# Optimization experiments

Measured on AMD Instinct MI355X. Metric: run time of the kernel, lower is better.

The kernel has to match this reference:

```python
import jax, jax.numpy as jnp
import numpy as np

DIM = 1024
NUM_HEADS = 16
HEAD_DIM = DIM // NUM_HEADS
ROPE_BASE = 10000.0


def apply_rope(x, pos):
    """x: [B, H, N, D] float32, pos: [B, N] int -> rotated x (rotate-half convention)."""
    d = x.shape[-1]
    # inv_freq: [D/2]
    inv_freq = 1.0 / (ROPE_BASE ** (jnp.arange(0, d, 2, dtype=jnp.float32) / d))
    # angles: [B, 1, N, D/2]
    ang = pos.astype(jnp.float32)[:, None, :, None] * inv_freq
    cos = jnp.concatenate([jnp.cos(ang), jnp.cos(ang)], axis=-1)
    sin = jnp.concatenate([jnp.sin(ang), jnp.sin(ang)], axis=-1)
    x1, x2 = x[..., : d // 2], x[..., d // 2 :]
    rotated = jnp.concatenate([-x2, x1], axis=-1)
    return x * cos + rotated * sin


def setup_inputs() -> dict:
    key = jax.random.key(0)
    ks = jax.random.split(key, 10)
    B, Nq, Nk, C = 4, 512, 2048, DIM
    scale = 0.02
    inp = {
        "query": jax.random.normal(ks[0], (B, Nq, C), dtype=jnp.float32),
        "key": jax.random.normal(ks[1], (B, Nk, C), dtype=jnp.float32),
        "value": jax.random.normal(ks[2], (B, Nk, C), dtype=jnp.float32),
        "qpos": jnp.sort(jax.random.randint(ks[3], (B, Nq), 0, Nk, dtype=jnp.int32), axis=-1),
        "kpos": jnp.sort(jax.random.randint(ks[4], (B, Nk), 0, Nk, dtype=jnp.int32), axis=-1),
        # learned params (qkv_bias=False; output proj has bias, per nn.Linear default)
        "Wq": jax.random.normal(ks[5], (C, C), dtype=jnp.float32) * scale,
        "Wk": jax.random.normal(ks[6], (C, C), dtype=jnp.float32) * scale,
        "Wv": jax.random.normal(ks[7], (C, C), dtype=jnp.float32) * scale,
        "Wp": jax.random.normal(ks[8], (C, C), dtype=jnp.float32) * scale,
        "bp": jax.random.normal(ks[9], (C,), dtype=jnp.float32) * scale,
    }
    return inp


def reference(query, key, value, qpos, kpos, Wq, Wk, Wv, Wp, bp):
    B, Nq, C = query.shape
    Nk = key.shape[1]
    H, D = NUM_HEADS, C // NUM_HEADS
    scale = D ** (-0.5)

    # separate Q/K/V linear projections (bias=False), split heads -> [B, H, N, D]
    q = (query @ Wq.T).reshape(B, Nq, H, D).transpose(0, 2, 1, 3)
    k = (key @ Wk.T).reshape(B, Nk, H, D).transpose(0, 2, 1, 3)
    v = (value @ Wv.T).reshape(B, Nk, H, D).transpose(0, 2, 1, 3)

    # RoPE applied in fp32 (matches the cast-to-float/rotate/cast-back sequence)
    q = apply_rope(q.astype(jnp.float32), qpos).astype(query.dtype)
    k = apply_rope(k.astype(jnp.float32), kpos).astype(key.dtype)

    # scaled dot-product attention (dropout_p = 0.0, non-causal)
    scores = jnp.einsum("bhqd,bhkd->bhqk", q, k) * scale
    attn = jax.nn.softmax(scores, axis=-1)
    x = jnp.einsum("bhqk,bhkd->bhqd", attn, v)

    # merge heads and output projection (with bias)
    x = x.transpose(0, 2, 1, 3).reshape(B, Nq, C)
    x = x @ Wp.T + bp
    return x
```

## Files before the change

### kernel.cpp

```cpp
#include <hip/hip_runtime.h>
#include <math.h>

#define B_ 4
#define NQ 512
#define NK 2048
#define C_ 1024
#define H_ 16
#define D_ 64
#define KK 1024

typedef __attribute__((ext_vector_type(8))) _Float16 half8;
typedef __attribute__((ext_vector_type(4))) _Float16 half4;
typedef __attribute__((ext_vector_type(4))) float float4v;

__device__ __forceinline__ void g2l16(const _Float16* g, _Float16* l)
{
    __builtin_amdgcn_global_load_lds(
        (const __attribute__((address_space(1))) unsigned int*)g,
        (__attribute__((address_space(3))) unsigned int*)l, 16, 0, 0);
}

__global__ __launch_bounds__(256) void cvt_w4(const float* __restrict__ W0,
                                              const float* __restrict__ W1,
                                              const float* __restrict__ W2,
                                              const float* __restrict__ W3,
                                              _Float16* __restrict__ W16)
{
    const int w = blockIdx.x >> 10, row = blockIdx.x & 1023;
    const float* src = (w == 0) ? W0 : (w == 1) ? W1 : (w == 2) ? W2 : W3;
    const int col = threadIdx.x * 4;
    float4 f = *(const float4*)(src + (size_t)row * 1024 + col);
    half4 h;
    h[0] = (_Float16)f.x; h[1] = (_Float16)f.y;
    h[2] = (_Float16)f.z; h[3] = (_Float16)f.w;
    *(half4*)(W16 + ((size_t)w << 20) + (size_t)row * 1024 + col) = h;
}

__global__ __launch_bounds__(256) void cvt_qkv(const float* __restrict__ q,
                                               const float* __restrict__ k,
                                               const float* __restrict__ v,
                                               _Float16* __restrict__ xq,
                                               _Float16* __restrict__ xk,
                                               _Float16* __restrict__ xv)
{
    const int blk = blockIdx.x;
    const float* src; _Float16* dst; int row;
    if (blk < 2048)       { src = q; dst = xq; row = blk; }
    else if (blk < 10240) { src = k; dst = xk; row = blk - 2048; }
    else                  { src = v; dst = xv; row = blk - 10240; }
    const int col = threadIdx.x * 4;
    float4 f = *(const float4*)(src + (size_t)row * 1024 + col);
    half4 h;
    h[0] = (_Float16)f.x; h[1] = (_Float16)f.y;
    h[2] = (_Float16)f.z; h[3] = (_Float16)f.w;
    *(half4*)(dst + (size_t)row * 1024 + col) = h;
}

__device__ __forceinline__ void gemm_body(const _Float16* __restrict__ A,
                                          const _Float16* __restrict__ Bw,
                                          _Float16* __restrict__ Yh,
                                          float* __restrict__ Yf,
                                          int mode, int nsh,
                                          const float* __restrict__ bias,
                                          _Float16* sA, _Float16* sB)
{
    const int tid = threadIdx.x;
    const int lane = tid & 63, wave = tid >> 6;
    const int n0 = blockIdx.x * 128, m0 = blockIdx.y * 128;
    const int wm = (wave >> 1) * 64, wn = (wave & 1) * 64;
    const int fm = lane & 15, quad = lane >> 4;

    const int srow = wave * 32 + (lane >> 3);
    const int soct = (lane & 7) ^ (srow & 7);
    const _Float16* gA = A  + (size_t)(m0 + srow) * KK + soct * 8;
    const _Float16* gB = Bw + (size_t)(n0 + srow) * KK + soct * 8;

    float4v acc[4][4];
    #pragma unroll
    for (int i = 0; i < 4; ++i)
        #pragma unroll
        for (int j = 0; j < 4; ++j)
            #pragma unroll
            for (int e = 0; e < 4; ++e) acc[i][j][e] = 0.0f;

    for (int k0 = 0; k0 < KK; k0 += 64) {
        __syncthreads();
        #pragma unroll
        for (int u = 0; u < 4; ++u) {
            g2l16(gA + (size_t)u * 8 * KK + k0, &sA[(wave * 32 + u * 8) * 64]);
            g2l16(gB + (size_t)u * 8 * KK + k0, &sB[(wave * 32 + u * 8) * 64]);
        }
        __syncthreads();

        #pragma unroll
        for (int ks = 0; ks < 2; ++ks) {
            const int po = ((ks * 4 + quad) ^ (fm & 7)) * 8;
            half8 a[4], b[4];
            #pragma unroll
            for (int i = 0; i < 4; ++i) {
                a[i] = *(const half8*)&sA[(wm + i * 16 + fm) * 64 + po];
                b[i] = *(const half8*)&sB[(wn + i * 16 + fm) * 64 + po];
            }
            #pragma unroll
            for (int i = 0; i < 4; ++i)
                #pragma unroll
                for (int j = 0; j < 4; ++j)
                    acc[i][j] = __builtin_amdgcn_mfma_f32_16x16x32_f16(a[i], b[j], acc[i][j], 0, 0, 0);
        }
    }

    const int rr = quad * 4;
    if (mode == 0) {
        const int nmask = (1 << nsh) - 1;
        #pragma unroll
        for (int i = 0; i < 4; ++i)
            #pragma unroll
            for (int r = 0; r < 4; ++r) {
                const int m = m0 + wm + i * 16 + rr + r;
                const int b = m >> nsh, n = m & nmask;
                #pragma unroll
                for (int j = 0; j < 4; ++j) {
                    const int c = n0 + wn + j * 16 + fm;
                    Yh[((((size_t)b * H_ + (c >> 6)) << nsh) + n) * 64 + (c & 63)] = (_Float16)acc[i][j][r];
                }
            }
    } else if (mode == 2) {
        const int nmask = (1 << nsh) - 1;
        #pragma unroll
        for (int i = 0; i < 4; ++i)
            #pragma unroll
            for (int r = 0; r < 4; ++r) {
                const int m = m0 + wm + i * 16 + rr + r;
                const int b = m >> nsh, n = m & nmask;
                #pragma unroll
                for (int j = 0; j < 4; ++j) {
                    const int c = n0 + wn + j * 16 + fm;
                    Yh[(((size_t)(b * H_ + (c >> 6)) * 64) + (c & 63)) * NK + n] = (_Float16)acc[i][j][r];
                }
            }
    } else {
        #pragma unroll
        for (int i = 0; i < 4; ++i)
            #pragma unroll
            for (int r = 0; r < 4; ++r) {
                const int m = m0 + wm + i * 16 + rr + r;
                #pragma unroll
                for (int j = 0; j < 4; ++j) {
                    const int c = n0 + wn + j * 16 + fm;
                    Yf[(size_t)m * 1024 + c] = acc[i][j][r] + bias[c];
                }
            }
    }
}

__global__ __launch_bounds__(256) void gemm_qkv(const _Float16* __restrict__ xq,
                                                const _Float16* __restrict__ xk,
                                                const _Float16* __restrict__ xv,
                                                const _Float16* __restrict__ W16,
                                                _Float16* __restrict__ qhp,
                                                _Float16* __restrict__ khp,
                                                _Float16* __restrict__ vtp)
{
    __shared__ _Float16 sA[128 * 64];
    __shared__ _Float16 sB[128 * 64];
    const int z = blockIdx.z;
    if (z == 0)
        gemm_body(xk, W16 + (1u << 20), khp, nullptr, 0, 11, nullptr, sA, sB);
    else if (z == 1)
        gemm_body(xv, W16 + (2u << 20), vtp, nullptr, 2, 11, nullptr, sA, sB);
    else {
        if (blockIdx.y >= 16) return;
        gemm_body(xq, W16, qhp, nullptr, 0, 9, nullptr, sA, sB);
    }
}

__global__ __launch_bounds__(256) void gemm_out(const _Float16* __restrict__ A,
                                                const _Float16* __restrict__ Bw,
                                                float* __restrict__ Yf,
                                                const float* __restrict__ bias)
{
    __shared__ _Float16 sA[128 * 64];
    __shared__ _Float16 sB[128 * 64];
    gemm_body(A, Bw, nullptr, Yf, 1, 0, bias, sA, sB);
}

__global__ __launch_bounds__(256) void rope_qk(_Float16* __restrict__ qh,
                                               _Float16* __restrict__ kh,
                                               const int* __restrict__ qpos,
                                               const int* __restrict__ kpos)
{
    int idx = blockIdx.x * 256 + threadIdx.x;
    const int QTOT = B_ * H_ * NQ * 32;
    _Float16* t; const int* pos; int Nseq; float scale;
    if (idx < QTOT) { t = qh; pos = qpos; Nseq = NQ; scale = 0.125f; }
    else { idx -= QTOT; t = kh; pos = kpos; Nseq = NK; scale = 1.0f; }

    const int i = idx & 31;
    const int n = (idx >> 5) % Nseq;
    const int b = (idx / (32 * Nseq)) >> 4;

    const double r = 0.74989420933245582;
    double f = 1.0;
    for (int u = 0; u < i; ++u) f *= r;

    const double ang = (double)pos[b * Nseq + n] * f;
    const double TWO_PI = 6.2831853071795864769;
    const float red = (float)(ang - TWO_PI * floor(ang / TWO_PI));
    float s, c;
    sincosf(red, &s, &c);

    const size_t base = ((size_t)(idx >> 5)) * 64 + i;
    const float x1 = (float)t[base];
    const float x2 = (float)t[base + 32];
    t[base]      = (_Float16)((x1 * c - x2 * s) * scale);
    t[base + 32] = (_Float16)((x2 * c + x1 * s) * scale);
}

__global__ __launch_bounds__(512) void attn_fused(const _Float16* __restrict__ qh,
                                                  const _Float16* __restrict__ kh,
                                                  const _Float16* __restrict__ vt,
                                                  _Float16* __restrict__ xw16)
{
    __shared__ _Float16 sK[2][64 * 64];
    __shared__ _Float16 sV[2][64 * 64];
    __shared__ _Float16 ps[8][16][66];

    const int tid = threadIdx.x;
    const int lane = tid & 63, wv = tid >> 6;
    const int bhi = blockIdx.x & 63;
    const int qquad = blockIdx.x >> 6;
    const size_t bh = (size_t)bhi;
    const int qt = qquad * 8 + wv;

    const int fm = lane & 15;
    const int quad = lane >> 4;
    const int fq = quad * 8;

    const _Float16* kb = kh + bh * NK * 64;
    const _Float16* vb = vt + bh * (size_t)64 * NK;

    const int r0 = lane >> 3;
    const int c4 = lane & 7;
    const int sch = c4 ^ r0;
    const _Float16* gK = kb + (size_t)(wv * 8 + r0) * 64 + sch * 8;
    const _Float16* gV = vb + (size_t)(wv * 8 + r0) * NK + sch * 8;

    const _Float16* qb = qh + (bh * NQ + (size_t)qt * 16) * 64;
    half8 aq[2];
    aq[0] = *(const half8*)(qb + (size_t)fm * 64 + fq);
    aq[1] = *(const half8*)(qb + (size_t)fm * 64 + 32 + fq);

    float l_acc[4] = {};
    float4v O[4];
    #pragma unroll
    for (int j = 0; j < 4; ++j)
        #pragma unroll
        for (int e = 0; e < 4; ++e) O[j][e] = 0.0f;

    const float4v z4 = {0.0f, 0.0f, 0.0f, 0.0f};

    g2l16(gK, &sK[0][wv * 512]);
    g2l16(gV, &sV[0][wv * 512]);
    __syncthreads();

    for (int it = 0; it < 32; ++it) {
        const int cur = it & 1;
        if (it < 31) {
            g2l16(gK + (size_t)(it + 1) * 64 * 64, &sK[cur ^ 1][wv * 512]);
            g2l16(gV + (it + 1) * 64,              &sV[cur ^ 1][wv * 512]);
        }
        const _Float16* Kc = sK[cur];
        const _Float16* Vc = sV[cur];

        half8 bk[4][2];
        #pragma unroll
        for (int j = 0; j < 4; ++j)
            #pragma unroll
            for (int ks = 0; ks < 2; ++ks)
                bk[j][ks] = *(const half8*)&Kc[(j * 16 + fm) * 64 + (((ks * 4 + quad) ^ (fm & 7)) * 8)];

        float4v s[4];
        __builtin_amdgcn_s_setprio(1);
        #pragma unroll
        for (int j = 0; j < 4; ++j) {
            s[j] = __builtin_amdgcn_mfma_f32_16x16x32_f16(aq[0], bk[j][0], z4, 0, 0, 0);
            s[j] = __builtin_amdgcn_mfma_f32_16x16x32_f16(aq[1], bk[j][1], s[j], 0, 0, 0);
        }
        __builtin_amdgcn_s_setprio(0);

        half8 bv[4][2];
        #pragma unroll
        for (int j = 0; j < 4; ++j)
            #pragma unroll
            for (int ks = 0; ks < 2; ++ks)
                bv[j][ks] = *(const half8*)&Vc[(j * 16 + fm) * 64 + (((ks * 4 + quad) ^ (fm & 7)) * 8)];

        #pragma unroll
        for (int j = 0; j < 4; ++j)
            #pragma unroll
            for (int r = 0; r < 4; ++r) {
                const float p = __expf(s[j][r]);
                l_acc[r] += p;
                ps[wv][quad * 4 + r][16 * j + fm] = (_Float16)p;
            }

        __builtin_amdgcn_s_setprio(1);
        #pragma unroll
        for (int ks = 0; ks < 2; ++ks) {
            half8 pa = *(const half8*)&ps[wv][fm][ks * 32 + fq];
            #pragma unroll
            for (int j = 0; j < 4; ++j)
                O[j] = __builtin_amdgcn_mfma_f32_16x16x32_f16(pa, bv[j][ks], O[j], 0, 0, 0);
        }
        __builtin_amdgcn_s_setprio(0);

        __syncthreads();
    }

    #pragma unroll
    for (int r = 0; r < 4; ++r) {
        float l = l_acc[r];
        l += __shfl_xor(l, 1);
        l += __shfl_xor(l, 2);
        l += __shfl_xor(l, 4);
        l += __shfl_xor(l, 8);
        const float inv = 1.0f / l;
        const int qr = quad * 4 + r;
        const int row = (bhi >> 4) * 512 + qt * 16 + qr;
        #pragma unroll
        for (int j = 0; j < 4; ++j) {
            const int col = (bhi & 15) * 64 + j * 16 + fm;
            xw16[(size_t)row * 1024 + col] = (_Float16)(O[j][r] * inv);
        }
    }
}

extern "C" void kernel_launch(void* const* d_in, const int* in_sizes, int n_in,
                              void* d_out, int out_size, void* d_ws, size_t ws_size,
                              hipStream_t stream)
{
    const float* query = (const float*)d_in[0];
    const float* key   = (const float*)d_in[1];
    const float* value = (const float*)d_in[2];
    const int*   qpos  = (const int*)d_in[3];
    const int*   kpos  = (const int*)d_in[4];
    const float* Wq    = (const float*)d_in[5];
    const float* Wk    = (const float*)d_in[6];
    const float* Wv    = (const float*)d_in[7];
    const float* Wp    = (const float*)d_in[8];
    const float* bp    = (const float*)d_in[9];
    float* out = (float*)d_out;

    char* ws = (char*)d_ws;
    _Float16* xk16  = (_Float16*)(ws);
    _Float16* xv16  = (_Float16*)(ws + (16u << 20));
    _Float16* xq16  = (_Float16*)(ws + (32u << 20));
    _Float16* W16   = (_Float16*)(ws + (36u << 20));
    _Float16* qhp   = (_Float16*)(ws + (44u << 20));
    _Float16* khp   = (_Float16*)(ws + (48u << 20));
    _Float16* vtp   = (_Float16*)(ws + (64u << 20));

    cvt_w4 <<<4096, 256, 0, stream>>>(Wq, Wk, Wv, Wp, W16);
    cvt_qkv<<<18432, 256, 0, stream>>>(query, key, value, xq16, xk16, xv16);

    gemm_qkv<<<dim3(8, 64, 3), 256, 0, stream>>>(xq16, xk16, xv16, W16, qhp, khp, vtp);

    rope_qk<<<(B_ * H_ * (NQ + NK) * 32) / 256, 256, 0, stream>>>(qhp, khp, qpos, kpos);

    attn_fused<<<256, 512, 0, stream>>>(qhp, khp, vtp, xq16);

    gemm_out<<<dim3(8, 16), 256, 0, stream>>>(xq16, W16 + (3u << 20), out, bp);
}
```

Baseline: 292.2 us.

## Rewrite QKV projection GEMM with 256x256 tiles and triple-buffered async LDS pipeline

```diff
diff --git a/kernel.cpp b/kernel.cpp
--- a/kernel.cpp
+++ b/kernel.cpp
@@ -56,64 +56,101 @@
     *(half4*)(dst + (size_t)row * 1024 + col) = h;
 }
 
-__device__ __forceinline__ void gemm_body(const _Float16* __restrict__ A,
-                                          const _Float16* __restrict__ Bw,
-                                          _Float16* __restrict__ Yh,
-                                          float* __restrict__ Yf,
-                                          int mode, int nsh,
-                                          const float* __restrict__ bias,
-                                          _Float16* sA, _Float16* sB)
-{
+__device__ __forceinline__ void stage_tile(const _Float16* gA, const _Float16* gB,
+                                           _Float16 (*sA)[8192], _Float16 (*sB)[8192],
+                                           int wv, int t, int bf)
+{
+    const size_t ko = (size_t)t * 32;
+    #pragma unroll
+    for (int u = 0; u < 2; ++u) {
+        g2l16(gA + (size_t)u * 16 * KK + ko, &sA[bf][(wv * 32 + u * 16) * 32]);
+        g2l16(gB + (size_t)u * 16 * KK + ko, &sB[bf][(wv * 32 + u * 16) * 32]);
+    }
+}
+
+__global__ __launch_bounds__(512) void gemm_qkv256(const _Float16* __restrict__ xq,
+                                                   const _Float16* __restrict__ xk,
+                                                   const _Float16* __restrict__ xv,
+                                                   const _Float16* __restrict__ W16,
+                                                   _Float16* __restrict__ qhp,
+                                                   _Float16* __restrict__ khp,
+                                                   _Float16* __restrict__ vtp)
+{
+    __shared__ _Float16 sA[3][8192];
+    __shared__ _Float16 sB[3][8192];
+
+    const int lbid = blockIdx.x;
+    const int xcd = lbid & 7, seq = lbid >> 3;
+    const int y = xcd + 8 * (seq >> 2);
+    const int n0 = (seq & 3) * 256;
+
+    const _Float16* A; const _Float16* Bw; _Float16* Yh;
+    int mode, nsh, m0;
+    if (y < 32)      { A = xk; Bw = W16 + (1u << 20); Yh = khp; mode = 0; nsh = 11; m0 = y * 256; }
+    else if (y < 64) { A = xv; Bw = W16 + (2u << 20); Yh = vtp; mode = 2; nsh = 11; m0 = (y - 32) * 256; }
+    else             { A = xq; Bw = W16;              Yh = qhp; mode = 0; nsh = 9;  m0 = (y - 64) * 256; }
+
     const int tid = threadIdx.x;
-    const int lane = tid & 63, wave = tid >> 6;
-    const int n0 = blockIdx.x * 128, m0 = blockIdx.y * 128;
-    const int wm = (wave >> 1) * 64, wn = (wave & 1) * 64;
+    const int lane = tid & 63, wv = tid >> 6;
+    const int wm = (wv >> 2) * 128, wn = (wv & 3) * 64;
     const int fm = lane & 15, quad = lane >> 4;
 
-    const int srow = wave * 32 + (lane >> 3);
-    const int soct = (lane & 7) ^ (srow & 7);
-    const _Float16* gA = A  + (size_t)(m0 + srow) * KK + soct * 8;
-    const _Float16* gB = Bw + (size_t)(n0 + srow) * KK + soct * 8;
-
-    float4v acc[4][4];
-    #pragma unroll
-    for (int i = 0; i < 4; ++i)
+    const int r0 = lane >> 2;
+    const int sch = (lane & 3) ^ (r0 & 3);
+    const _Float16* gA = A  + (size_t)(m0 + wv * 32 + r0) * KK + sch * 8;
+    const _Float16* gB = Bw + (size_t)(n0 + wv * 32 + r0) * KK + sch * 8;
+
+    float4v acc[8][4];
+    #pragma unroll
+    for (int i = 0; i < 8; ++i)
         #pragma unroll
         for (int j = 0; j < 4; ++j)
             #pragma unroll
             for (int e = 0; e < 4; ++e) acc[i][j][e] = 0.0f;
 
-    for (int k0 = 0; k0 < KK; k0 += 64) {
-        __syncthreads();
-        #pragma unroll
-        for (int u = 0; u < 4; ++u) {
-            g2l16(gA + (size_t)u * 8 * KK + k0, &sA[(wave * 32 + u * 8) * 64]);
-            g2l16(gB + (size_t)u * 8 * KK + k0, &sB[(wave * 32 + u * 8) * 64]);
-        }
-        __syncthreads();
-
-        #pragma unroll
-        for (int ks = 0; ks < 2; ++ks) {
-            const int po = ((ks * 4 + quad) ^ (fm & 7)) * 8;
-            half8 a[4], b[4];
-            #pragma unroll
-            for (int i = 0; i < 4; ++i) {
-                a[i] = *(const half8*)&sA[(wm + i * 16 + fm) * 64 + po];
-                b[i] = *(const half8*)&sB[(wn + i * 16 + fm) * 64 + po];
-            }
-            #pragma unroll
-            for (int i = 0; i < 4; ++i)
-                #pragma unroll
-                for (int j = 0; j < 4; ++j)
-                    acc[i][j] = __builtin_amdgcn_mfma_f32_16x16x32_f16(a[i], b[j], acc[i][j], 0, 0, 0);
-        }
+    stage_tile(gA, gB, sA, sB, wv, 0, 0);
+    stage_tile(gA, gB, sA, sB, wv, 1, 1);
+
+    const int po = (quad ^ (fm & 3)) * 8;
+
+    for (int t = 0; t < 32; ++t) {
+        const int bf = t % 3;
+        if (t + 2 < 32)
+            stage_tile(gA, gB, sA, sB, wv, t + 2, (t + 2) % 3);
+
+        if (t < 30)       asm volatile("s_waitcnt vmcnt(8)" ::: "memory");
+        else if (t == 30) asm volatile("s_waitcnt vmcnt(4)" ::: "memory");
+        else              asm volatile("s_waitcnt vmcnt(0)" ::: "memory");
+        __builtin_amdgcn_sched_barrier(0);
+        __builtin_amdgcn_s_barrier();
+        __builtin_amdgcn_sched_barrier(0);
+
+        half8 b[4];
+        #pragma unroll
+        for (int j = 0; j < 4; ++j)
+            b[j] = *(const half8*)&sB[bf][(wn + j * 16 + fm) * 32 + po];
+
+        __builtin_amdgcn_s_setprio(1);
+        #pragma unroll
+        for (int i = 0; i < 8; ++i) {
+            half8 ai = *(const half8*)&sA[bf][(wm + i * 16 + fm) * 32 + po];
+            #pragma unroll
+            for (int j = 0; j < 4; ++j)
+                acc[i][j] = __builtin_amdgcn_mfma_f32_16x16x32_f16(ai, b[j], acc[i][j], 0, 0, 0);
+        }
+        __builtin_amdgcn_s_setprio(0);
+
+        asm volatile("s_waitcnt lgkmcnt(0)" ::: "memory");
+        __builtin_amdgcn_sched_barrier(0);
+        __builtin_amdgcn_s_barrier();
+        __builtin_amdgcn_sched_barrier(0);
     }
 
     const int rr = quad * 4;
     if (mode == 0) {
         const int nmask = (1 << nsh) - 1;
         #pragma unroll
-        for (int i = 0; i < 4; ++i)
+        for (int i = 0; i < 8; ++i)
             #pragma unroll
             for (int r = 0; r < 4; ++r) {
                 const int m = m0 + wm + i * 16 + rr + r;
@@ -124,10 +161,10 @@
                     Yh[((((size_t)b * H_ + (c >> 6)) << nsh) + n) * 64 + (c & 63)] = (_Float16)acc[i][j][r];
                 }
             }
-    } else if (mode == 2) {
+    } else {
         const int nmask = (1 << nsh) - 1;
         #pragma unroll
-        for (int i = 0; i < 4; ++i)
+        for (int i = 0; i < 8; ++i)
             #pragma unroll
             for (int r = 0; r < 4; ++r) {
                 const int m = m0 + wm + i * 16 + rr + r;
@@ -138,40 +175,72 @@
                     Yh[(((size_t)(b * H_ + (c >> 6)) * 64) + (c & 63)) * NK + n] = (_Float16)acc[i][j][r];
                 }
             }
-    } else {
-        #pragma unroll
-        for (int i = 0; i < 4; ++i)
-            #pragma unroll
-            for (int r = 0; r < 4; ++r) {
-                const int m = m0 + wm + i * 16 + rr + r;
+    }
+}
+
+__device__ __forceinline__ void gemm_body(const _Float16* __restrict__ A,
+                                          const _Float16* __restrict__ Bw,
+                                          float* __restrict__ Yf,
+                                          const float* __restrict__ bias,
+                                          _Float16* sA, _Float16* sB)
+{
+    const int tid = threadIdx.x;
+    const int lane = tid & 63, wave = tid >> 6;
+    const int n0 = blockIdx.x * 128, m0 = blockIdx.y * 128;
+    const int wm = (wave >> 1) * 64, wn = (wave & 1) * 64;
+    const int fm = lane & 15, quad = lane >> 4;
+
+    const int srow = wave * 32 + (lane >> 3);
+    const int soct = (lane & 7) ^ (srow & 7);
+    const _Float16* gA = A  + (size_t)(m0 + srow) * KK + soct * 8;
+    const _Float16* gB = Bw + (size_t)(n0 + srow) * KK + soct * 8;
+
+    float4v acc[4][4];
+    #pragma unroll
+    for (int i = 0; i < 4; ++i)
+        #pragma unroll
+        for (int j = 0; j < 4; ++j)
+            #pragma unroll
+            for (int e = 0; e < 4; ++e) acc[i][j][e] = 0.0f;
+
+    for (int k0 = 0; k0 < KK; k0 += 64) {
+        __syncthreads();
+        #pragma unroll
+        for (int u = 0; u < 4; ++u) {
+            g2l16(gA + (size_t)u * 8 * KK + k0, &sA[(wave * 32 + u * 8) * 64]);
+            g2l16(gB + (size_t)u * 8 * KK + k0, &sB[(wave * 32 + u * 8) * 64]);
+        }
+        __syncthreads();
+
+        #pragma unroll
+        for (int ks = 0; ks < 2; ++ks) {
+            const int po = ((ks * 4 + quad) ^ (fm & 7)) * 8;
+            half8 a[4], b[4];
+            #pragma unroll
+            for (int i = 0; i < 4; ++i) {
+                a[i] = *(const half8*)&sA[(wm + i * 16 + fm) * 64 + po];
+                b[i] = *(const half8*)&sB[(wn + i * 16 + fm) * 64 + po];
+            }
+            #pragma unroll
+            for (int i = 0; i < 4; ++i)
                 #pragma unroll
-                for (int j = 0; j < 4; ++j) {
-                    const int c = n0 + wn + j * 16 + fm;
-                    Yf[(size_t)m * 1024 + c] = acc[i][j][r] + bias[c];
-                }
+                for (int j = 0; j < 4; ++j)
+                    acc[i][j] = __builtin_amdgcn_mfma_f32_16x16x32_f16(a[i], b[j], acc[i][j], 0, 0, 0);
+        }
+    }
+
+    const int rr = quad * 4;
+    #pragma unroll
+    for (int i = 0; i < 4; ++i)
+        #pragma unroll
+        for (int r = 0; r < 4; ++r) {
+            const int m = m0 + wm + i * 16 + rr + r;
+            #pragma unroll
+            for (int j = 0; j < 4; ++j) {
+                const int c = n0 + wn + j * 16 + fm;
+                Yf[(size_t)m * 1024 + c] = acc[i][j][r] + bias[c];
             }
-    }
-}
-
-__global__ __launch_bounds__(256) void gemm_qkv(const _Float16* __restrict__ xq,
-                                                const _Float16* __restrict__ xk,
-                                                const _Float16* __restrict__ xv,
-                                                const _Float16* __restrict__ W16,
-                                                _Float16* __restrict__ qhp,
-                                                _Float16* __restrict__ khp,
-                                                _Float16* __restrict__ vtp)
-{
-    __shared__ _Float16 sA[128 * 64];
-    __shared__ _Float16 sB[128 * 64];
-    const int z = blockIdx.z;
-    if (z == 0)
-        gemm_body(xk, W16 + (1u << 20), khp, nullptr, 0, 11, nullptr, sA, sB);
-    else if (z == 1)
-        gemm_body(xv, W16 + (2u << 20), vtp, nullptr, 2, 11, nullptr, sA, sB);
-    else {
-        if (blockIdx.y >= 16) return;
-        gemm_body(xq, W16, qhp, nullptr, 0, 9, nullptr, sA, sB);
-    }
+        }
 }
 
 __global__ __launch_bounds__(256) void gemm_out(const _Float16* __restrict__ A,
@@ -181,7 +250,7 @@
 {
     __shared__ _Float16 sA[128 * 64];
     __shared__ _Float16 sB[128 * 64];
-    gemm_body(A, Bw, nullptr, Yf, 1, 0, bias, sA, sB);
+    gemm_body(A, Bw, Yf, bias, sA, sB);
 }
 
 __global__ __launch_bounds__(256) void rope_qk(_Float16* __restrict__ qh,
@@ -199,13 +268,17 @@
     const int n = (idx >> 5) % Nseq;
     const int b = (idx / (32 * Nseq)) >> 4;
 
-    const double r = 0.74989420933245582;
     double f = 1.0;
-    for (int u = 0; u < i; ++u) f *= r;
+    if (i & 1)  f *= 0.7498942093324559;
+    if (i & 2)  f *= 0.5623413251903491;
+    if (i & 4)  f *= 0.31622776601683794;
+    if (i & 8)  f *= 0.1;
+    if (i & 16) f *= 0.01;
 
     const double ang = (double)pos[b * Nseq + n] * f;
     const double TWO_PI = 6.2831853071795864769;
-    const float red = (float)(ang - TWO_PI * floor(ang / TWO_PI));
+    const double INV_TWO_PI = 0.15915494309189533577;
+    const float red = (float)(ang - TWO_PI * floor(ang * INV_TWO_PI));
     float s, c;
     sincosf(red, &s, &c);
 
@@ -363,7 +436,7 @@
     cvt_w4 <<<4096, 256, 0, stream>>>(Wq, Wk, Wv, Wp, W16);
     cvt_qkv<<<18432, 256, 0, stream>>>(query, key, value, xq16, xk16, xv16);
 
-    gemm_qkv<<<dim3(8, 64, 3), 256, 0, stream>>>(xq16, xk16, xv16, W16, qhp, khp, vtp);
+    gemm_qkv256<<<288, 512, 0, stream>>>(xq16, xk16, xv16, W16, qhp, khp, vtp);
 
     rope_qk<<<(B_ * H_ * (NQ + NK) * 32) / 256, 256, 0, stream>>>(qhp, khp, qpos, kpos);
 
```

Result: no change. 293.8 us (+0.5%).
